# Kernel tuning notes

Measured on AMD Instinct MI355X. Metric: run time of the kernel, lower is better.

The kernel has to match this reference:

```python
import jax, jax.numpy as jnp
import numpy as np

EMBED = 2048
HEADS = 16
HEAD_DIM = EMBED // HEADS


def setup_inputs() -> dict:
    key = jax.random.key(0)
    ks = jax.random.split(key, 9)
    B, S, E = 4, 2048, EMBED
    scale = 1.0 / np.sqrt(E)
    return {
        "values": jax.random.normal(ks[0], (B, S, E), jnp.float32),
        "keys": jax.random.normal(ks[1], (B, S, E), jnp.float32),
        "query": jax.random.normal(ks[2], (B, S, E), jnp.float32),
        "mask": jax.random.randint(ks[3], (1, 1, S, S), 0, 2, jnp.int32),
        "Wv": jax.random.normal(ks[4], (E, E), jnp.float32) * scale,
        "Wk": jax.random.normal(ks[5], (E, E), jnp.float32) * scale,
        "Wq": jax.random.normal(ks[6], (E, E), jnp.float32) * scale,
        "Wo": jax.random.normal(ks[7], (E, E), jnp.float32) * scale,
        "bo": jax.random.normal(ks[8], (E,), jnp.float32) * 0.01,
    }


def reference(values, keys, query, mask, Wv, Wk, Wq, Wo, bo):
    N, q_len, E = query.shape
    # QKV projections (no bias)
    v = jnp.matmul(values, Wv)
    k = jnp.matmul(keys, Wk)
    q = jnp.matmul(query, Wq)
    # [N, len, E] -> [N, heads, len, head_dim]
    def split_heads(x):
        return jnp.transpose(x.reshape(N, x.shape[1], HEADS, HEAD_DIM), (0, 2, 1, 3))
    v, k, q = split_heads(v), split_heads(k), split_heads(q)
    # scaled dot-product attention: [N, H, q_len, k_len]
    energy = jnp.einsum("bhqd,bhkd->bhqk", q, k) / jnp.sqrt(jnp.float32(HEAD_DIM))
    energy = jnp.where(mask == 0, jnp.float32(-1e20), energy)
    attn = jax.nn.softmax(energy, axis=-1)
    out = jnp.einsum("bhqk,bhkd->bhqd", attn, v)
    out = jnp.transpose(out, (0, 2, 1, 3)).reshape(N, q_len, E)
    return jnp.matmul(out, Wo) + bo
```

## Files before the change

### kernel.cpp

```cpp
#include <hip/hip_runtime.h>
#include <hip/hip_bf16.h>
#include <stdint.h>
#include <math.h>

#define EMB   2048
#define NH    16
#define HD    128
#define BATCH 4
#define SEQ   2048

typedef __bf16 bf16_t;
typedef __bf16 bf16x8 __attribute__((ext_vector_type(8)));
typedef __bf16 bf16x4 __attribute__((ext_vector_type(4)));
typedef float  f32x4  __attribute__((ext_vector_type(4)));
typedef float  f32x16 __attribute__((ext_vector_type(16)));

__device__ inline void gload_lds16(const void* g, void* l) {
  __builtin_amdgcn_global_load_lds(
      (const __attribute__((address_space(1))) uint32_t*)g,
      (__attribute__((address_space(3))) uint32_t*)l, 16, 0, 0);
}

__device__ inline uint32_t pack_bf2(float a, float b) {
  uint16_t lo = __builtin_bit_cast(uint16_t, (bf16_t)a);
  uint16_t hi = __builtin_bit_cast(uint16_t, (bf16_t)b);
  return (uint32_t)lo | ((uint32_t)hi << 16);
}

__device__ inline float ex2(float x) {
#if __has_builtin(__builtin_amdgcn_exp2f)
  return __builtin_amdgcn_exp2f(x);
#else
  float r; asm volatile("v_exp_f32 %0, %1" : "=v"(r) : "v"(x)); return r;
#endif
}

__device__ inline uint32_t sext1(uint32_t x, int b) {
  return (uint32_t)(((int32_t)(x << (31 - b))) >> 31);
}
__device__ inline float andf(float p, uint32_t m) {
  return __builtin_bit_cast(float, __builtin_bit_cast(uint32_t, p) & m);
}


__global__ __launch_bounds__(256) void conv_bf16(const float* __restrict__ x,
                                                 bf16_t* __restrict__ y) {
  size_t t = (size_t)blockIdx.x * 256 + threadIdx.x;
  float4 v = ((const float4*)x)[t];
  bf16x4 o;
  o[0] = (bf16_t)v.x; o[1] = (bf16_t)v.y; o[2] = (bf16_t)v.z; o[3] = (bf16_t)v.w;
  ((bf16x4*)y)[t] = o;
}

__global__ __launch_bounds__(256) void convT_w(const float* __restrict__ W,
                                               bf16_t* __restrict__ Wt) {
  __shared__ float t[32][33];
  int tx = threadIdx.x & 31, ty = threadIdx.x >> 5;
  int nb = blockIdx.x * 32, kb = blockIdx.y * 32;
#pragma unroll
  for (int i = 0; i < 4; ++i)
    t[ty + 8 * i][tx] = W[(size_t)(kb + ty + 8 * i) * EMB + nb + tx];
  __syncthreads();
#pragma unroll
  for (int i = 0; i < 4; ++i)
    Wt[(size_t)(nb + ty + 8 * i) * EMB + kb + tx] = (bf16_t)t[tx][ty + 8 * i];
}

__global__ __launch_bounds__(256) void pack_mask(const int* __restrict__ mask,
                                                 uint32_t* __restrict__ maskb) {
  int t = blockIdx.x * 256 + threadIdx.x;
  int q = t >> 6, w = t & 63;
  const int* row = mask + (size_t)q * SEQ + w * 32;
  uint32_t acc = 0;
#pragma unroll 8
  for (int i = 0; i < 32; ++i) acc |= (row[i] != 0 ? 1u : 0u) << i;
  maskb[t] = acc;
}

template <int MODE>
__global__ __launch_bounds__(256) void gemm128(const bf16_t* __restrict__ A,
                                               const bf16_t* __restrict__ Bt,
                                               bf16_t* __restrict__ outb,
                                               float* __restrict__ outf,
                                               const float* __restrict__ bias) {
  __shared__ bf16_t As[128 * 32];
  __shared__ bf16_t Bs[128 * 32];
  const int tid = threadIdx.x;
  const int wid = tid >> 6, lane = tid & 63;
  const int wr = wid >> 1, wc = wid & 1;
  const int m0 = blockIdx.y * 128, n0 = blockIdx.x * 128;

  f32x4 acc[4][4] = {};

  const int sr = lane >> 2;
  const int scs = ((lane & 3) ^ (sr & 3)) * 8;
  const int ia0 = wid * 2;

  for (int kt = 0; kt < EMB / 32; ++kt) {
    const int k0 = kt * 32;
#pragma unroll
    for (int j = 0; j < 2; ++j) {
      int i = ia0 + j;
      int r = i * 16 + sr;
      gload_lds16(&A[(size_t)(m0 + r) * EMB + k0 + scs], &As[i * 512]);
      gload_lds16(&Bt[(size_t)(n0 + r) * EMB + k0 + scs], &Bs[i * 512]);
    }
    asm volatile("s_waitcnt vmcnt(0)" ::: "memory");
    __syncthreads();

    const int fr = lane & 15;
    const int fks = ((lane >> 4) ^ (fr & 3)) * 8;
    bf16x8 af[4], bfr[4];
#pragma unroll
    for (int mf = 0; mf < 4; ++mf)
      af[mf] = *(const bf16x8*)&As[(wr * 64 + mf * 16 + fr) * 32 + fks];
#pragma unroll
    for (int nf = 0; nf < 4; ++nf)
      bfr[nf] = *(const bf16x8*)&Bs[(wc * 64 + nf * 16 + fr) * 32 + fks];
#pragma unroll
    for (int mf = 0; mf < 4; ++mf)
#pragma unroll
      for (int nf = 0; nf < 4; ++nf) {
        if (MODE == 1)
          acc[mf][nf] = __builtin_amdgcn_mfma_f32_16x16x32_bf16(bfr[nf], af[mf],
                                                                acc[mf][nf], 0, 0, 0);
        else
          acc[mf][nf] = __builtin_amdgcn_mfma_f32_16x16x32_bf16(af[mf], bfr[nf],
                                                                acc[mf][nf], 0, 0, 0);
      }
    __syncthreads();
  }

  const int col0 = lane & 15;
  const int row0 = (lane >> 4) * 4;
#pragma unroll
  for (int mf = 0; mf < 4; ++mf) {
#pragma unroll
    for (int r = 0; r < 4; ++r) {
#pragma unroll
      for (int nf = 0; nf < 4; ++nf) {
        float v = acc[mf][nf][r];
        if (MODE == 1) {
          int nr = n0 + wc * 64 + nf * 16 + row0 + r;
          int mc = m0 + wr * 64 + mf * 16 + col0;
          int b = mc >> 11, s = mc & 2047, h = nr >> 7, d = nr & 127;
          outb[((size_t)(b * NH + h) * HD + d) * SEQ + s] = (bf16_t)v;
        } else {
          int m = m0 + wr * 64 + mf * 16 + row0 + r;
          int n = n0 + wc * 64 + nf * 16 + col0;
          if (MODE == 0) {
            int b = m >> 11, s = m & 2047, h = n >> 7, d = n & 127;
            outb[((size_t)(b * NH + h) * SEQ + s) * HD + d] = (bf16_t)v;
          } else {
            outf[(size_t)m * EMB + n] = v + bias[n];
          }
        }
      }
    }
  }
}

__global__ __launch_bounds__(256, 2) void attn_fwd(const bf16_t* __restrict__ Q,
                                                   const bf16_t* __restrict__ K,
                                                   const bf16_t* __restrict__ Vt,
                                                   const uint32_t* __restrict__ maskb,
                                                   bf16_t* __restrict__ O) {
  __shared__ bf16_t Ks[2][64 * 128];
  __shared__ bf16_t Vs[2][128 * 64];
  const int tid = threadIdx.x;
  const int wid = tid >> 6, lane = tid & 63;
  const int ln = lane & 31, hi = lane >> 5;
  const int bid = blockIdx.x;
  const int slot = bid >> 3;
  const int bh = (bid & 7) * 8 + (slot >> 4);
  const int qt = slot & 15;
  const int b = bh >> 4, h = bh & 15;
  const int q = qt * 128 + wid * 32 + ln;
  const float C2 = 0.08838834764831845f * 1.4426950408889634f;

  bf16x8 qf[8];
  const bf16_t* qrow = Q + ((size_t)bh * SEQ + q) * HD;
#pragma unroll
  for (int ks = 0; ks < 8; ++ks)
    qf[ks] = *(const bf16x8*)&qrow[ks * 16 + hi * 8];

  const bf16_t* kp[8];
  const bf16_t* vp[4];
#pragma unroll
  for (int ks = 0; ks < 8; ++ks)
    kp[ks] = &Ks[0][ln * 128 + (((2 * ks + hi) ^ (ln & 7)) * 8)];
#pragma unroll
  for (int ks = 0; ks < 4; ++ks)
    vp[ks] = &Vs[0][ln * 64 + (((2 * ks + hi) ^ (ln & 7)) * 8)];

  f32x16 oacc[4] = {};
  float mC = -INFINITY, l_run = 0.f;

  const size_t kbase = (size_t)bh * SEQ * HD;
  const size_t vbase = (size_t)bh * HD * SEQ;
  const uint2* mb = (const uint2*)maskb;

#define STAGE(BUF, KT)                                                          \
  do {                                                                          \
    const int _k0 = (KT) * 64;                                                  \
    _Pragma("unroll")                                                           \
    for (int j = 0; j < 4; ++j) {                                               \
      int i = wid * 4 + j;                                                      \
      { int r = i * 4 + (lane >> 4); int c = lane & 15;                         \
        gload_lds16(&K[kbase + (size_t)(_k0 + r) * HD + ((c ^ (r & 7)) * 8)],   \
                    &Ks[BUF][i * 512]); }                                       \
      { int r = i * 8 + (lane >> 3); int c = lane & 7;                          \
        gload_lds16(&Vt[vbase + (size_t)r * SEQ + _k0 + ((c ^ (r & 7)) * 8)],   \
                    &Vs[BUF][i * 512]); }                                       \
    }                                                                           \
  } while (0)

  const int NT = SEQ / 64;
  uint2 mw_cur = mb[(size_t)q * 32];
  uint2 mw_next;
  STAGE(0, 0);

#define TILE(KT, P)                                                             \
  {                                                                             \
    asm volatile("s_waitcnt vmcnt(0)" ::: "memory");  \
    asm volatile("s_barrier" ::: "memory");           \
    if ((KT) + 1 < NT) {                                                        \
      mw_next = mb[(size_t)q * 32 + (KT) + 1];           \
      STAGE((P) ^ 1, (KT) + 1);                                                 \
    }                                                                           \
    f32x16 sacc0 = {}, sacc1 = {};                                              \
    __builtin_amdgcn_s_setprio(1);                                              \
    _Pragma("unroll")                                                           \
    for (int ks = 0; ks < 8; ++ks) {                                            \
      bf16x8 kf0 = *(const bf16x8*)(kp[ks] + (P) * 8192);                       \
      bf16x8 kf1 = *(const bf16x8*)(kp[ks] + 4096 + (P) * 8192);                \
      sacc0 = __builtin_amdgcn_mfma_f32_32x32x16_bf16(kf0, qf[ks], sacc0, 0, 0, 0); \
      sacc1 = __builtin_amdgcn_mfma_f32_32x32x16_bf16(kf1, qf[ks], sacc1, 0, 0, 0); \
    }                                                                           \
    __builtin_amdgcn_s_setprio(0);                                              \
    const uint32_t mwx = mw_cur.x >> (4 * hi);                                  \
    const uint32_t mwy = mw_cur.y >> (4 * hi);                                  \
    float pmax = -INFINITY;                                                     \
    _Pragma("unroll")                                                           \
    for (int r = 0; r < 16; r += 4)                                             \
      pmax = fmaxf(pmax, fmaxf(fmaxf(sacc0[r], sacc0[r + 1]),                   \
                               fmaxf(sacc0[r + 2], sacc0[r + 3])));             \
    _Pragma("unroll")                                                           \
    for (int r = 0; r < 16; r += 4)                                             \
      pmax = fmaxf(pmax, fmaxf(fmaxf(sacc1[r], sacc1[r + 1]),                   \
                               fmaxf(sacc1[r + 2], sacc1[r + 3])));             \
    pmax = fmaxf(pmax, __shfl_xor(pmax, 32, 64));                               \
    const float pmaxC = pmax * C2;                                              \
    if (!__all(pmaxC - mC <= 8.0f)) {                                           \
      const float mnewC = fmaxf(mC, pmaxC);                                     \
      const float corr = ex2(mC - mnewC);                                       \
      _Pragma("unroll")                                                         \
      for (int mv = 0; mv < 4; ++mv)                                            \
        _Pragma("unroll")                                                       \
        for (int r = 0; r < 16; ++r) oacc[mv][r] *= corr;                       \
      l_run *= corr;                                                            \
      mC = mnewC;                                                               \
    }                                                                           \
    const float nmC = -mC;                                                      \
    float psum = 0.f;                                                           \
    uint32_t pk[2][4][2];                                                       \
    _Pragma("unroll")                                                           \
    for (int g = 0; g < 4; ++g) {                                               \
      float p0 = andf(ex2(fmaf(sacc0[4 * g + 0], C2, nmC)), sext1(mwx, 8 * g + 0)); \
      float p1 = andf(ex2(fmaf(sacc0[4 * g + 1], C2, nmC)), sext1(mwx, 8 * g + 1)); \
      float p2 = andf(ex2(fmaf(sacc0[4 * g + 2], C2, nmC)), sext1(mwx, 8 * g + 2)); \
      float p3 = andf(ex2(fmaf(sacc0[4 * g + 3], C2, nmC)), sext1(mwx, 8 * g + 3)); \
      psum += (p0 + p1) + (p2 + p3);                                            \
      pk[0][g][0] = pack_bf2(p0, p1);                                           \
      pk[0][g][1] = pack_bf2(p2, p3);                                           \
      float q0 = andf(ex2(fmaf(sacc1[4 * g + 0], C2, nmC)), sext1(mwy, 8 * g + 0)); \
      float q1 = andf(ex2(fmaf(sacc1[4 * g + 1], C2, nmC)), sext1(mwy, 8 * g + 1)); \
      float q2 = andf(ex2(fmaf(sacc1[4 * g + 2], C2, nmC)), sext1(mwy, 8 * g + 2)); \
      float q3 = andf(ex2(fmaf(sacc1[4 * g + 3], C2, nmC)), sext1(mwy, 8 * g + 3)); \
      psum += (q0 + q1) + (q2 + q3);                                            \
      pk[1][g][0] = pack_bf2(q0, q1);                                           \
      pk[1][g][1] = pack_bf2(q2, q3);                                           \
    }                                                                           \
    psum += __shfl_xor(psum, 32, 64);                                           \
    l_run += psum;                                                              \
    _Pragma("unroll")                                                           \
    for (int ks = 0; ks < 4; ++ks) {                                            \
      const int mfp = ks >> 1;                                                  \
      const int gA = (2 * ks) & 3;                                              \
      uint32_t w0 = pk[mfp][gA][0], w1 = pk[mfp][gA][1];                        \
      uint32_t w2 = pk[mfp][gA + 1][0], w3 = pk[mfp][gA + 1][1];                \
      asm("v_permlane32_swap_b32 %0, %1" : "+v"(w0), "+v"(w2));                 \
      asm("v_permlane32_swap_b32 %0, %1" : "+v"(w1), "+v"(w3));                 \
      uint4 bw = make_uint4(w0, w1, w2, w3);                                    \
      bf16x8 pb = __builtin_bit_cast(bf16x8, bw);                               \
      __builtin_amdgcn_s_setprio(1);                                            \
      _Pragma("unroll")                                                         \
      for (int mv = 0; mv < 4; ++mv) {                                          \
        bf16x8 vf = *(const bf16x8*)(vp[ks] + mv * 2048 + (P) * 8192);          \
        oacc[mv] = __builtin_amdgcn_mfma_f32_32x32x16_bf16(vf, pb, oacc[mv], 0, 0, 0); \
      }                                                                         \
      __builtin_amdgcn_s_setprio(0);                                            \
    }                                                                           \
    mw_cur = mw_next;                                                           \
  }

  for (int t = 0; t < NT; t += 2) {
    TILE(t, 0);
    TILE(t + 1, 1);
  }
#undef TILE
#undef STAGE

  const float invl = 1.f / l_run;
  bf16_t* orow = O + ((size_t)b * SEQ + q) * EMB + h * HD;
#pragma unroll
  for (int mv = 0; mv < 4; ++mv) {
#pragma unroll
    for (int g = 0; g < 4; ++g) {
      int d = mv * 32 + 8 * g + 4 * hi;
      bf16x4 ov;
      ov[0] = (bf16_t)(oacc[mv][4 * g + 0] * invl);
      ov[1] = (bf16_t)(oacc[mv][4 * g + 1] * invl);
      ov[2] = (bf16_t)(oacc[mv][4 * g + 2] * invl);
      ov[3] = (bf16_t)(oacc[mv][4 * g + 3] * invl);
      *(bf16x4*)&orow[d] = ov;
    }
  }
}


extern "C" void kernel_launch(void* const* d_in, const int* in_sizes, int n_in,
                              void* d_out, int out_size, void* d_ws, size_t ws_size,
                              hipStream_t stream) {
  const float* values = (const float*)d_in[0];
  const float* keys   = (const float*)d_in[1];
  const float* query  = (const float*)d_in[2];
  const int*   mask   = (const int*)d_in[3];
  const float* Wv = (const float*)d_in[4];
  const float* Wk = (const float*)d_in[5];
  const float* Wq = (const float*)d_in[6];
  const float* Wo = (const float*)d_in[7];
  const float* bo = (const float*)d_in[8];
  float* out = (float*)d_out;

  char* ws = (char*)d_ws;
  bf16_t*   Xbuf  = (bf16_t*)(ws);
  bf16_t*   Wbuf  = (bf16_t*)(ws + 33554432);
  bf16_t*   Qb    = (bf16_t*)(ws + 41943040);
  bf16_t*   Kb    = (bf16_t*)(ws + 75497472);
  bf16_t*   Vtb   = (bf16_t*)(ws + 109051904);
  uint32_t* maskb = (uint32_t*)(ws + 142606336);

  dim3 b256(256);
  dim3 gconv(16384);
  dim3 gw(64, 64);
  dim3 gg(16, 64);
  dim3 ga(1024);

  pack_mask<<<dim3(512), b256, 0, stream>>>(mask, maskb);

  conv_bf16<<<gconv, b256, 0, stream>>>(query, Xbuf);
  convT_w<<<gw, b256, 0, stream>>>(Wq, Wbuf);
  gemm128<0><<<gg, b256, 0, stream>>>(Xbuf, Wbuf, Qb, nullptr, nullptr);

  conv_bf16<<<gconv, b256, 0, stream>>>(keys, Xbuf);
  convT_w<<<gw, b256, 0, stream>>>(Wk, Wbuf);
  gemm128<0><<<gg, b256, 0, stream>>>(Xbuf, Wbuf, Kb, nullptr, nullptr);

  conv_bf16<<<gconv, b256, 0, stream>>>(values, Xbuf);
  convT_w<<<gw, b256, 0, stream>>>(Wv, Wbuf);
  gemm128<1><<<gg, b256, 0, stream>>>(Xbuf, Wbuf, Vtb, nullptr, nullptr);

  attn_fwd<<<ga, b256, 0, stream>>>(Qb, Kb, Vtb, maskb, Xbuf);

  convT_w<<<gw, b256, 0, stream>>>(Wo, Wbuf);
  gemm128<2><<<gg, b256, 0, stream>>>(Xbuf, Wbuf, nullptr, out, bo);
}
```

Before: 655.1 us.

## Replace 128x128 GEMM with 256x256-tile double-buffered 512-thread GEMM

Replaces the projection GEMM, which used 128x128 tiles, K=32 steps and a single LDS buffer, with a 256x256-tile kernel. The new kernel uses 8 waves, K=64 steps and double-buffered dynamic LDS (128KB), staging tile t+2 while computing tile t, and splits the MFMA work into four phases with explicit barriers and priority hints. The intent is more data reuse per loaded byte and overlap of global loads with compute. The trade-offs are fewer blocks (256, one per CU), heavy LDS and register use, and more per-call host attribute calls.

New measurement: 554.8 us (median of 2 runs). -15.3%, faster.

```diff
diff --git a/kernel.cpp b/kernel.cpp
--- a/kernel.cpp
+++ b/kernel.cpp
@@ -77,77 +77,135 @@
   maskb[t] = acc;
 }
 
+#define KTILES (EMB / 64)
+
 template <int MODE>
-__global__ __launch_bounds__(256) void gemm128(const bf16_t* __restrict__ A,
-                                               const bf16_t* __restrict__ Bt,
-                                               bf16_t* __restrict__ outb,
-                                               float* __restrict__ outf,
-                                               const float* __restrict__ bias) {
-  __shared__ bf16_t As[128 * 32];
-  __shared__ bf16_t Bs[128 * 32];
+__global__ __launch_bounds__(512, 2) void gemm256(const bf16_t* __restrict__ A,
+                                                  const bf16_t* __restrict__ Bt,
+                                                  bf16_t* __restrict__ outb,
+                                                  float* __restrict__ outf,
+                                                  const float* __restrict__ bias) {
+  extern __shared__ bf16_t lds[];
   const int tid = threadIdx.x;
   const int wid = tid >> 6, lane = tid & 63;
-  const int wr = wid >> 1, wc = wid & 1;
-  const int m0 = blockIdx.y * 128, n0 = blockIdx.x * 128;
-
-  f32x4 acc[4][4] = {};
-
-  const int sr = lane >> 2;
-  const int scs = ((lane & 3) ^ (sr & 3)) * 8;
-  const int ia0 = wid * 2;
-
-  for (int kt = 0; kt < EMB / 32; ++kt) {
-    const int k0 = kt * 32;
-#pragma unroll
-    for (int j = 0; j < 2; ++j) {
-      int i = ia0 + j;
-      int r = i * 16 + sr;
-      gload_lds16(&A[(size_t)(m0 + r) * EMB + k0 + scs], &As[i * 512]);
-      gload_lds16(&Bt[(size_t)(n0 + r) * EMB + k0 + scs], &Bs[i * 512]);
-    }
-    asm volatile("s_waitcnt vmcnt(0)" ::: "memory");
-    __syncthreads();
-
-    const int fr = lane & 15;
-    const int fks = ((lane >> 4) ^ (fr & 3)) * 8;
-    bf16x8 af[4], bfr[4];
-#pragma unroll
-    for (int mf = 0; mf < 4; ++mf)
-      af[mf] = *(const bf16x8*)&As[(wr * 64 + mf * 16 + fr) * 32 + fks];
-#pragma unroll
-    for (int nf = 0; nf < 4; ++nf)
-      bfr[nf] = *(const bf16x8*)&Bs[(wc * 64 + nf * 16 + fr) * 32 + fks];
-#pragma unroll
-    for (int mf = 0; mf < 4; ++mf)
-#pragma unroll
-      for (int nf = 0; nf < 4; ++nf) {
-        if (MODE == 1)
-          acc[mf][nf] = __builtin_amdgcn_mfma_f32_16x16x32_bf16(bfr[nf], af[mf],
-                                                                acc[mf][nf], 0, 0, 0);
-        else
-          acc[mf][nf] = __builtin_amdgcn_mfma_f32_16x16x32_bf16(af[mf], bfr[nf],
-                                                                acc[mf][nf], 0, 0, 0);
-      }
-    __syncthreads();
+  const int wr = wid >> 2;
+  const int wcn = wid & 3;
+  const int tn = blockIdx.x & 7;
+  const int tm = blockIdx.x >> 3;
+  const int m0 = tm * 256, n0 = tn * 256;
+
+  f32x4 acc[8][4] = {};
+  bf16x8 af[4][2], bfrg[2][2];
+
+  const int trow = tid >> 3;
+  const int schunk = ((tid & 7) ^ (trow & 7)) * 8;
+  const int fr = lane & 15;
+  const int l7 = lane & 7;
+  const int hi4 = lane >> 4;
+  int cslot[2];
+  cslot[0] = ((hi4) ^ l7) * 8;
+  cslot[1] = ((4 + hi4) ^ l7) * 8;
+  const int arow = wr * 128 + fr;
+  const int brow = wcn * 64 + fr;
+
+#define STAGE_HALF(DST, SRC)                                                    \
+  do {                                                                          \
+    gload_lds16((SRC), &lds[(DST) + wid * 512]);                                \
+    gload_lds16((SRC) + (size_t)64 * EMB, &lds[(DST) + wid * 512 + 4096]);      \
+  } while (0)
+
+#define STAGE_TILE(B, KT)                                                       \
+  do {                                                                          \
+    const bf16_t* _a = A + (size_t)(m0 + trow) * EMB + (KT) * 64 + schunk;      \
+    STAGE_HALF((B) * 16384, _a);                                                \
+    STAGE_HALF((B) * 16384 + 8192, _a + (size_t)128 * EMB);                     \
+    const bf16_t* _b = Bt + (size_t)(n0 + trow) * EMB + (KT) * 64 + schunk;     \
+    STAGE_HALF(32768 + (B) * 16384, _b);                                        \
+    STAGE_HALF(32768 + (B) * 16384 + 8192, _b + (size_t)128 * EMB);             \
+  } while (0)
+
+#define READ_A(P, QM)                                                           \
+  _Pragma("unroll") for (int i = 0; i < 4; ++i)                                 \
+  _Pragma("unroll") for (int ks = 0; ks < 2; ++ks)                              \
+    af[i][ks] = *(const bf16x8*)&lds[(P) * 16384 +                              \
+                    (arow + ((QM) * 4 + i) * 16) * 64 + cslot[ks]];
+
+#define READ_B(P, QN)                                                           \
+  _Pragma("unroll") for (int j = 0; j < 2; ++j)                                 \
+  _Pragma("unroll") for (int ks = 0; ks < 2; ++ks)                              \
+    bfrg[j][ks] = *(const bf16x8*)&lds[32768 + (P) * 16384 +                    \
+                    (brow + ((QN) * 2 + j) * 16) * 64 + cslot[ks]];
+
+#define PHASE(P, QM, QN, DO_A)                                                  \
+  do {                                                                          \
+    if (DO_A) { READ_A(P, QM); }                                                \
+    READ_B(P, QN);                                                              \
+    asm volatile("s_barrier" ::: "memory");                                     \
+    asm volatile("s_waitcnt lgkmcnt(0)" ::: "memory");                          \
+    __builtin_amdgcn_sched_barrier(0);                                          \
+    __builtin_amdgcn_s_setprio(1);                                              \
+    _Pragma("unroll") for (int i = 0; i < 4; ++i)                               \
+    _Pragma("unroll") for (int j = 0; j < 2; ++j)                               \
+    _Pragma("unroll") for (int ks = 0; ks < 2; ++ks) {                          \
+      if (MODE == 1)                                                            \
+        acc[(QM) * 4 + i][(QN) * 2 + j] = __builtin_amdgcn_mfma_f32_16x16x32_bf16( \
+            bfrg[j][ks], af[i][ks], acc[(QM) * 4 + i][(QN) * 2 + j], 0, 0, 0);  \
+      else                                                                      \
+        acc[(QM) * 4 + i][(QN) * 2 + j] = __builtin_amdgcn_mfma_f32_16x16x32_bf16( \
+            af[i][ks], bfrg[j][ks], acc[(QM) * 4 + i][(QN) * 2 + j], 0, 0, 0);  \
+    }                                                                           \
+    __builtin_amdgcn_s_setprio(0);                                              \
+    asm volatile("s_barrier" ::: "memory");                                     \
+  } while (0)
+
+#define ITER(T, P)                                                              \
+  do {                                                                          \
+    PHASE(P, 0, 0, 1);                                                          \
+    PHASE(P, 0, 1, 0);                                                          \
+    PHASE(P, 1, 0, 1);                                                          \
+    PHASE(P, 1, 1, 0);                                                          \
+    if ((T) + 2 < KTILES) {                                                     \
+      STAGE_TILE(P, (T) + 2);                                                   \
+      asm volatile("s_waitcnt vmcnt(8)" ::: "memory");                          \
+    } else {                                                                    \
+      asm volatile("s_waitcnt vmcnt(0)" ::: "memory");                          \
+    }                                                                           \
+    asm volatile("s_barrier" ::: "memory");                                     \
+  } while (0)
+
+  STAGE_TILE(0, 0);
+  STAGE_TILE(1, 1);
+  asm volatile("s_waitcnt vmcnt(8)" ::: "memory");
+  asm volatile("s_barrier" ::: "memory");
+
+  for (int t = 0; t < KTILES; t += 2) {
+    ITER(t, 0);
+    ITER(t + 1, 1);
   }
+#undef ITER
+#undef PHASE
+#undef READ_B
+#undef READ_A
+#undef STAGE_TILE
+#undef STAGE_HALF
 
   const int col0 = lane & 15;
   const int row0 = (lane >> 4) * 4;
 #pragma unroll
-  for (int mf = 0; mf < 4; ++mf) {
+  for (int mf = 0; mf < 8; ++mf) {
 #pragma unroll
     for (int r = 0; r < 4; ++r) {
 #pragma unroll
       for (int nf = 0; nf < 4; ++nf) {
         float v = acc[mf][nf][r];
         if (MODE == 1) {
-          int nr = n0 + wc * 64 + nf * 16 + row0 + r;
-          int mc = m0 + wr * 64 + mf * 16 + col0;
+          int nr = n0 + wcn * 64 + nf * 16 + row0 + r;
+          int mc = m0 + wr * 128 + mf * 16 + col0;
           int b = mc >> 11, s = mc & 2047, h = nr >> 7, d = nr & 127;
           outb[((size_t)(b * NH + h) * HD + d) * SEQ + s] = (bf16_t)v;
         } else {
-          int m = m0 + wr * 64 + mf * 16 + row0 + r;
-          int n = n0 + wc * 64 + nf * 16 + col0;
+          int m = m0 + wr * 128 + mf * 16 + row0 + r;
+          int n = n0 + wcn * 64 + nf * 16 + col0;
           if (MODE == 0) {
             int b = m >> 11, s = m & 2047, h = n >> 7, d = n & 127;
             outb[((size_t)(b * NH + h) * SEQ + s) * HD + d] = (bf16_t)v;
@@ -222,10 +280,10 @@
 
 #define TILE(KT, P)                                                             \
   {                                                                             \
-    asm volatile("s_waitcnt vmcnt(0)" ::: "memory");  \
-    asm volatile("s_barrier" ::: "memory");           \
+    asm volatile("s_waitcnt vmcnt(0)" ::: "memory");                            \
+    asm volatile("s_barrier" ::: "memory");                                     \
     if ((KT) + 1 < NT) {                                                        \
-      mw_next = mb[(size_t)q * 32 + (KT) + 1];           \
+      mw_next = mb[(size_t)q * 32 + (KT) + 1];                                  \
       STAGE((P) ^ 1, (KT) + 1);                                                 \
     }                                                                           \
     f32x16 sacc0 = {}, sacc1 = {};                                              \
@@ -351,28 +409,36 @@
   bf16_t*   Vtb   = (bf16_t*)(ws + 109051904);
   uint32_t* maskb = (uint32_t*)(ws + 142606336);
 
-  dim3 b256(256);
+  static const size_t GEMM_LDS = 131072;
+  hipFuncSetAttribute(reinterpret_cast<const void*>(gemm256<0>),
+                      hipFuncAttributeMaxDynamicSharedMemorySize, (int)GEMM_LDS);
+  hipFuncSetAttribute(reinterpret_cast<const void*>(gemm256<1>),
+                      hipFuncAttributeMaxDynamicSharedMemorySize, (int)GEMM_LDS);
+  hipFuncSetAttribute(reinterpret_cast<const void*>(gemm256<2>),
+                      hipFuncAttributeMaxDynamicSharedMemorySize, (int)GEMM_LDS);
+
+  dim3 b256(256), b512(512);
   dim3 gconv(16384);
   dim3 gw(64, 64);
-  dim3 gg(16, 64);
+  dim3 gg(256);
   dim3 ga(1024);
 
   pack_mask<<<dim3(512), b256, 0, stream>>>(mask, maskb);
 
   conv_bf16<<<gconv, b256, 0, stream>>>(query, Xbuf);
   convT_w<<<gw, b256, 0, stream>>>(Wq, Wbuf);
-  gemm128<0><<<gg, b256, 0, stream>>>(Xbuf, Wbuf, Qb, nullptr, nullptr);
+  gemm256<0><<<gg, b512, GEMM_LDS, stream>>>(Xbuf, Wbuf, Qb, nullptr, nullptr);
 
   conv_bf16<<<gconv, b256, 0, stream>>>(keys, Xbuf);
   convT_w<<<gw, b256, 0, stream>>>(Wk, Wbuf);
-  gemm128<0><<<gg, b256, 0, stream>>>(Xbuf, Wbuf, Kb, nullptr, nullptr);
+  gemm256<0><<<gg, b512, GEMM_LDS, stream>>>(Xbuf, Wbuf, Kb, nullptr, nullptr);
 
   conv_bf16<<<gconv, b256, 0, stream>>>(values, Xbuf);
   convT_w<<<gw, b256, 0, stream>>>(Wv, Wbuf);
-  gemm128<1><<<gg, b256, 0, stream>>>(Xbuf, Wbuf, Vtb, nullptr, nullptr);
+  gemm256<1><<<gg, b512, GEMM_LDS, stream>>>(Xbuf, Wbuf, Vtb, nullptr, nullptr);
 
   attn_fwd<<<ga, b256, 0, stream>>>(Qb, Kb, Vtb, maskb, Xbuf);
 
   convT_w<<<gw, b256, 0, stream>>>(Wo, Wbuf);
-  gemm128<2><<<gg, b256, 0, stream>>>(Xbuf, Wbuf, nullptr, out, bo);
-}
+  gemm256<2><<<gg, b512, GEMM_LDS, stream>>>(Xbuf, Wbuf, nullptr, out, bo);
+}
```
